# Kernel tuning notes

Hardware: AMD Instinct MI355X
Metric: run time of the kernel (lower is better)

Reference implementation:

```python
import jax, jax.numpy as jnp
import numpy as np

E = 1024      # d_model
H = 16        # num heads
D = E // H    # head dim = 64
FF = 4096     # dim_feedforward
WIN = 128
EPS = 1e-5    # layer-norm eps
NEG = -1e9


def setup_inputs() -> dict:
    key = jax.random.key(0)
    ks = jax.random.split(key, 16)
    s = 0.02
    f32 = jnp.float32
    return {
        "src":       jax.random.normal(ks[0], (2, 2048, E), f32),
        "in_proj_w": jax.random.normal(ks[1], (3 * E, E), f32) * s,
        "in_proj_b": jnp.zeros((3 * E,), f32),
        "out_w":     jax.random.normal(ks[2], (E, E), f32) * s,
        "out_b":     jnp.zeros((E,), f32),
        "lin1_w":    jax.random.normal(ks[3], (FF, E), f32) * s,
        "lin1_b":    jnp.zeros((FF,), f32),
        "lin2_w":    jax.random.normal(ks[4], (E, FF), f32) * s,
        "lin2_b":    jnp.zeros((E,), f32),
        "ln1_g":     jnp.ones((E,), f32),
        "ln1_beta":  jnp.zeros((E,), f32),
        "ln2_g":     jnp.ones((E,), f32),
        "ln2_beta":  jnp.zeros((E,), f32),
    }


def _layer_norm(x, g, b):
    mu = x.mean(-1, keepdims=True)
    var = ((x - mu) ** 2).mean(-1, keepdims=True)
    return (x - mu) * jax.lax.rsqrt(var + EPS) * g + b


def reference(src, in_proj_w, in_proj_b, out_w, out_b,
              lin1_w, lin1_b, lin2_w, lin2_b,
              ln1_g, ln1_beta, ln2_g, ln2_beta):
    B, L, _ = src.shape  # batch_first=True
    x = src

    # fused QKV projection (torch Linear: y = x @ W.T + b)
    qkv = x @ in_proj_w.T + in_proj_b            # [B, L, 3E]
    q, k, v = jnp.split(qkv, 3, axis=-1)
    q = q.reshape(B, L, H, D)
    k = k.reshape(B, L, H, D)
    v = v.reshape(B, L, H, D)

    scores = jnp.einsum('blhd,bmhd->bhlm', q, k) / np.float32(np.sqrt(D))
    idx = jnp.arange(L)
    band = jnp.abs(idx[:, None] - idx[None, :]) <= WIN   # [L, L] allowed positions
    scores = jnp.where(band, scores, NEG)
    attn = jax.nn.softmax(scores, axis=-1)

    ctx = jnp.einsum('bhlm,bmhd->blhd', attn, v).reshape(B, L, E)
    attn_out = ctx @ out_w.T + out_b

    # post-norm transformer encoder layer (norm_first=False default)
    x = _layer_norm(x + attn_out, ln1_g, ln1_beta)
    ff = jax.nn.relu(x @ lin1_w.T + lin1_b) @ lin2_w.T + lin2_b
    return _layer_norm(x + ff, ln2_g, ln2_beta)
```

## Files before the change

### kernel.cpp

```cpp
#include <hip/hip_runtime.h>
#include <cstdint>
#include <cstddef>


typedef __attribute__((ext_vector_type(8))) short short8;
typedef __attribute__((ext_vector_type(4))) float f32x4;

__device__ __forceinline__ float b2f(unsigned short u) {
  union { unsigned int i; float f; } x; x.i = ((unsigned int)u) << 16; return x.f;
}
__device__ __forceinline__ unsigned short f2b(float f) {
  union { float f; unsigned int i; } x; x.f = f;
  unsigned int i = x.i;
  unsigned int r = (i + 0x7FFFu + ((i >> 16) & 1u)) >> 16;
  return (unsigned short)r;
}
__device__ __forceinline__ uint4 pack8(float4 f0, float4 f1) {
  uint4 r;
  r.x = (unsigned)f2b(f0.x) | ((unsigned)f2b(f0.y) << 16);
  r.y = (unsigned)f2b(f0.z) | ((unsigned)f2b(f0.w) << 16);
  r.z = (unsigned)f2b(f1.x) | ((unsigned)f2b(f1.y) << 16);
  r.w = (unsigned)f2b(f1.z) | ((unsigned)f2b(f1.w) << 16);
  return r;
}

__device__ __forceinline__ void gl_lds16(const unsigned short* g, unsigned short* l) {
  __builtin_amdgcn_global_load_lds(
      (const __attribute__((address_space(1))) unsigned int*)g,
      (__attribute__((address_space(3))) unsigned int*)l, 16, 0, 0);
}

__global__ __launch_bounds__(256) void conv_k(
    const float* __restrict__ in, unsigned short* __restrict__ out, int n)
{
  const int i = (blockIdx.x * 256 + threadIdx.x) * 8;
  if (i < n) {
    const float4 f0 = *(const float4*)(in + i);
    const float4 f1 = *(const float4*)(in + i + 4);
    *(uint4*)(out + i) = pack8(f0, f1);
  }
}

__global__ __launch_bounds__(256) void conv3_k(
    const float* __restrict__ src, unsigned short* __restrict__ srcb,
    const float* __restrict__ w_in, const float* __restrict__ w_out,
    unsigned short* __restrict__ wslot)
{
  const int i = (blockIdx.x * 256 + threadIdx.x) * 8;
  const float* in;
  unsigned short* out;
  if (i < 4194304)      { in = src + i;                 out = srcb + i; }
  else if (i < 7340032) { in = w_in + (i - 4194304);    out = wslot + (i - 4194304); }
  else                  { in = w_out + (i - 7340032);   out = wslot + (i - 4194304); }
  const float4 f0 = *(const float4*)(in);
  const float4 f1 = *(const float4*)(in + 4);
  *(uint4*)(out) = pack8(f0, f1);
}

template<int RELU, int OUT32>
__global__ __launch_bounds__(512, 2) void gemm256(
    const unsigned short* __restrict__ A, const unsigned short* __restrict__ Wb,
    const float* __restrict__ bias, void* __restrict__ out,
    int M, int N, int K)
{
  __shared__ unsigned short As[2][256 * 64];
  __shared__ unsigned short Bs[2][256 * 64];

  const int tid = threadIdx.x;
  const int lane = tid & 63, wid = tid >> 6;
  const int wm = wid >> 2, wn = wid & 3;

  const int gx = gridDim.x;
  const int flat = blockIdx.y * gx + blockIdx.x;
  const int chunk = (gx * gridDim.y) >> 3;
  const int nf = (flat & 7) * chunk + (flat >> 3);
  const int m0 = (nf / gx) * 256, n0 = (nf % gx) * 256;

  int offA[2][2], offB[2][2], ldsO2[2][2];
#pragma unroll
  for (int h1 = 0; h1 < 2; ++h1)
#pragma unroll
    for (int i = 0; i < 2; ++i) {
      const int sl = i * 512 + tid;
      const int r = h1 * 128 + (sl >> 3);
      const int sslot = sl & 7;
      const int c = (sslot + r) & 7;
      offA[h1][i] = (m0 + r) * K + c * 8;
      offB[h1][i] = (n0 + r) * K + c * 8;
      ldsO2[h1][i] = (h1 * 1024 + i * 512 + (tid & ~63)) * 8;
    }

  const int cl = lane & 15;
  const int kg = lane >> 4;

  int aoff[4][2], boff[2][2];
#pragma unroll
  for (int mt = 0; mt < 4; ++mt) {
    const int ar = wm * 64 + mt * 16 + cl;
#pragma unroll
    for (int ks = 0; ks < 2; ++ks)
      aoff[mt][ks] = ar * 64 + (((ks * 4 + kg) - ar) & 7) * 8;
  }
#pragma unroll
  for (int nt = 0; nt < 2; ++nt) {
    const int br = wn * 32 + nt * 16 + cl;
#pragma unroll
    for (int ks = 0; ks < 2; ++ks)
      boff[nt][ks] = br * 64 + (((ks * 4 + kg) - br) & 7) * 8;
  }

  f32x4 acc[8][4];
#pragma unroll
  for (int i = 0; i < 8; ++i)
#pragma unroll
    for (int j = 0; j < 4; ++j) acc[i][j] = (f32x4){0.f, 0.f, 0.f, 0.f};

  const int steps = K >> 6;

#define STAGE256(idx_) do { const int _x = (idx_); if (_x < 4 * steps) {        \
    const int T_ = _x >> 2, j_ = _x & 3, bf_ = T_ & 1; const int ko = T_ << 6;  \
    if (j_ == 0)      { gl_lds16(A  + offA[0][0] + ko, &As[bf_][ldsO2[0][0]]);  \
                        gl_lds16(A  + offA[0][1] + ko, &As[bf_][ldsO2[0][1]]); }\
    else if (j_ == 1) { gl_lds16(Wb + offB[0][0] + ko, &Bs[bf_][ldsO2[0][0]]);  \
                        gl_lds16(Wb + offB[0][1] + ko, &Bs[bf_][ldsO2[0][1]]); }\
    else if (j_ == 2) { gl_lds16(Wb + offB[1][0] + ko, &Bs[bf_][ldsO2[1][0]]);  \
                        gl_lds16(Wb + offB[1][1] + ko, &Bs[bf_][ldsO2[1][1]]); }\
    else              { gl_lds16(A  + offA[1][0] + ko, &As[bf_][ldsO2[1][0]]);  \
                        gl_lds16(A  + offA[1][1] + ko, &As[bf_][ldsO2[1][1]]); }\
  } } while (0)

  STAGE256(0); STAGE256(1); STAGE256(2); STAGE256(3);
  STAGE256(4); STAGE256(5); STAGE256(6);
  asm volatile("s_waitcnt vmcnt(6)" ::: "memory");
  __builtin_amdgcn_s_barrier();

  int cur = 0;
  for (int s = 0; s < steps; ++s) {
    short8 bf0[2][2], af[4][2];
#pragma unroll
    for (int nt = 0; nt < 2; ++nt)
#pragma unroll
      for (int ks = 0; ks < 2; ++ks) bf0[nt][ks] = *(const short8*)&Bs[cur][boff[nt][ks]];
#pragma unroll
    for (int mt = 0; mt < 4; ++mt)
#pragma unroll
      for (int ks = 0; ks < 2; ++ks) af[mt][ks] = *(const short8*)&As[cur][aoff[mt][ks]];
    STAGE256(4 * s + 7);
    asm volatile("s_waitcnt lgkmcnt(8)" ::: "memory");
    __builtin_amdgcn_s_barrier();
    asm volatile("s_waitcnt lgkmcnt(0)" ::: "memory");
    __builtin_amdgcn_sched_barrier(0);
    __builtin_amdgcn_s_setprio(1);
#pragma unroll
    for (int mt = 0; mt < 4; ++mt)
#pragma unroll
      for (int nt = 0; nt < 2; ++nt)
#pragma unroll
        for (int ks = 0; ks < 2; ++ks)
          acc[mt][nt] = __builtin_amdgcn_mfma_f32_16x16x32_bf16(af[mt][ks], bf0[nt][ks], acc[mt][nt], 0, 0, 0);
    __builtin_amdgcn_s_setprio(0);
    __builtin_amdgcn_s_barrier();

    short8 bf1[2][2];
#pragma unroll
    for (int nt = 0; nt < 2; ++nt)
#pragma unroll
      for (int ks = 0; ks < 2; ++ks) bf1[nt][ks] = *(const short8*)&Bs[cur][boff[nt][ks] + 8192];
    STAGE256(4 * s + 8);
    __builtin_amdgcn_s_barrier();
    asm volatile("s_waitcnt lgkmcnt(0)" ::: "memory");
    __builtin_amdgcn_sched_barrier(0);
    __builtin_amdgcn_s_setprio(1);
#pragma unroll
    for (int mt = 0; mt < 4; ++mt)
#pragma unroll
      for (int nt = 0; nt < 2; ++nt)
#pragma unroll
        for (int ks = 0; ks < 2; ++ks)
          acc[mt][nt + 2] = __builtin_amdgcn_mfma_f32_16x16x32_bf16(af[mt][ks], bf1[nt][ks], acc[mt][nt + 2], 0, 0, 0);
    __builtin_amdgcn_s_setprio(0);
    __builtin_amdgcn_s_barrier();

    short8 ag[4][2];
#pragma unroll
    for (int mt = 0; mt < 4; ++mt)
#pragma unroll
      for (int ks = 0; ks < 2; ++ks) ag[mt][ks] = *(const short8*)&As[cur][aoff[mt][ks] + 8192];
    STAGE256(4 * s + 9);
    __builtin_amdgcn_s_barrier();
    asm volatile("s_waitcnt lgkmcnt(0)" ::: "memory");
    __builtin_amdgcn_sched_barrier(0);
    __builtin_amdgcn_s_setprio(1);
#pragma unroll
    for (int mt = 0; mt < 4; ++mt)
#pragma unroll
      for (int nt = 0; nt < 2; ++nt)
#pragma unroll
        for (int ks = 0; ks < 2; ++ks)
          acc[mt + 4][nt] = __builtin_amdgcn_mfma_f32_16x16x32_bf16(ag[mt][ks], bf0[nt][ks], acc[mt + 4][nt], 0, 0, 0);
    __builtin_amdgcn_s_setprio(0);
    __builtin_amdgcn_s_barrier();

    STAGE256(4 * s + 10);
    if (s < steps - 2)       asm volatile("s_waitcnt vmcnt(6)" ::: "memory");
    else if (s == steps - 2) asm volatile("s_waitcnt vmcnt(0)" ::: "memory");
    __builtin_amdgcn_s_barrier();
    __builtin_amdgcn_s_setprio(1);
#pragma unroll
    for (int mt = 0; mt < 4; ++mt)
#pragma unroll
      for (int nt = 0; nt < 2; ++nt)
#pragma unroll
        for (int ks = 0; ks < 2; ++ks)
          acc[mt + 4][nt + 2] = __builtin_amdgcn_mfma_f32_16x16x32_bf16(ag[mt][ks], bf1[nt][ks], acc[mt + 4][nt + 2], 0, 0, 0);
    __builtin_amdgcn_s_setprio(0);
    __builtin_amdgcn_s_barrier();

    cur ^= 1;
  }
#undef STAGE256

#pragma unroll
  for (int nt = 0; nt < 4; ++nt) {
    const int colB = wn * 32 + (nt & 1) * 16 + (nt >> 1) * 128;
    const int col = n0 + colB + cl;
    const float bvs = bias[col];
#pragma unroll
    for (int mt = 0; mt < 8; ++mt) {
      const int rowA = wm * 64 + (mt & 3) * 16 + (mt >> 2) * 128;
#pragma unroll
      for (int r = 0; r < 4; ++r) {
        const int grow = m0 + rowA + kg * 4 + r;
        float v = acc[mt][nt][r] + bvs;
        if (RELU) v = fmaxf(v, 0.f);
        if (OUT32) ((float*)out)[(size_t)grow * N + col] = v;
        else       ((unsigned short*)out)[(size_t)grow * N + col] = f2b(v);
      }
    }
  }
}

template<int OUT32>
__global__ __launch_bounds__(256) void gemm64(
    const unsigned short* __restrict__ A, const unsigned short* __restrict__ Wb,
    const float* __restrict__ bias, void* __restrict__ out,
    int M, int N, int K)
{
  __shared__ unsigned short As[3][64 * 64];
  __shared__ unsigned short Bs[3][128 * 64];

  const int tid = threadIdx.x;
  const int lane = tid & 63, wid = tid >> 6;

  const int nwgx = gridDim.x;
  const int flat = blockIdx.y * nwgx + blockIdx.x;
  const int chunk = (nwgx * gridDim.y) >> 3;
  const int nf = (flat & 7) * chunk + (flat >> 3);
  const int m0 = (nf / nwgx) * 64, n0 = (nf % nwgx) * 128;

  const unsigned short* gA[2];
  const unsigned short* gW[4];
  int ldsA[2], ldsB[4];
#pragma unroll
  for (int i = 0; i < 2; ++i) {
    const int sl = wid * 128 + i * 64 + lane;
    const int r = sl >> 3, s = sl & 7, c = (s + r) & 7;
    gA[i] = A + (size_t)(m0 + r) * K + c * 8;
    ldsA[i] = (wid * 128 + i * 64) * 8;
  }
#pragma unroll
  for (int i = 0; i < 4; ++i) {
    const int sl = wid * 256 + i * 64 + lane;
    const int r = sl >> 3, s = sl & 7, c = (s + r) & 7;
    gW[i] = Wb + (size_t)(n0 + r) * K + c * 8;
    ldsB[i] = (wid * 256 + i * 64) * 8;
  }

  const int cl = lane & 15;
  const int kg = lane >> 4;
  int aoff[4][2], boff[2][2];
#pragma unroll
  for (int t = 0; t < 4; ++t) {
    const int ar = t * 16 + cl;
#pragma unroll
    for (int ks = 0; ks < 2; ++ks)
      aoff[t][ks] = ar * 64 + ((ks * 4 + kg - ar) & 7) * 8;
  }
#pragma unroll
  for (int t = 0; t < 2; ++t) {
    const int br = wid * 32 + t * 16 + cl;
#pragma unroll
    for (int ks = 0; ks < 2; ++ks)
      boff[t][ks] = br * 64 + ((ks * 4 + kg - br) & 7) * 8;
  }

  f32x4 acc[4][2];
#pragma unroll
  for (int i = 0; i < 4; ++i)
#pragma unroll
    for (int j = 0; j < 2; ++j) acc[i][j] = (f32x4){0.f, 0.f, 0.f, 0.f};

  const int steps = K >> 6;

  const int pre = steps < 3 ? steps : 3;
  for (int t = 0; t < pre; ++t) {
#pragma unroll
    for (int i = 0; i < 2; ++i) { gl_lds16(gA[i], &As[t][ldsA[i]]); gA[i] += 64; }
#pragma unroll
    for (int i = 0; i < 4; ++i) { gl_lds16(gW[i], &Bs[t][ldsB[i]]); gW[i] += 64; }
  }

  int cur = 0;
  for (int s = 0; s < steps; ++s) {
    const int rem = steps - 1 - s;
    if (rem >= 2)      asm volatile("s_waitcnt vmcnt(12)" ::: "memory");
    else if (rem == 1) asm volatile("s_waitcnt vmcnt(6)" ::: "memory");
    else               asm volatile("s_waitcnt vmcnt(0)" ::: "memory");
    __builtin_amdgcn_s_barrier();

    short8 af[4][2], bf[2][2];
#pragma unroll
    for (int t = 0; t < 4; ++t)
#pragma unroll
      for (int ks = 0; ks < 2; ++ks) af[t][ks] = *(const short8*)&As[cur][aoff[t][ks]];
#pragma unroll
    for (int t = 0; t < 2; ++t)
#pragma unroll
      for (int ks = 0; ks < 2; ++ks) bf[t][ks] = *(const short8*)&Bs[cur][boff[t][ks]];

    asm volatile("s_waitcnt lgkmcnt(0)" ::: "memory");
    __builtin_amdgcn_sched_barrier(0);
    __builtin_amdgcn_s_barrier();

    if (s + 3 < steps) {
#pragma unroll
      for (int i = 0; i < 2; ++i) { gl_lds16(gA[i], &As[cur][ldsA[i]]); gA[i] += 64; }
#pragma unroll
      for (int i = 0; i < 4; ++i) { gl_lds16(gW[i], &Bs[cur][ldsB[i]]); gW[i] += 64; }
    }

#pragma unroll
    for (int mt = 0; mt < 4; ++mt)
#pragma unroll
      for (int nt = 0; nt < 2; ++nt)
#pragma unroll
        for (int ks = 0; ks < 2; ++ks)
          acc[mt][nt] = __builtin_amdgcn_mfma_f32_16x16x32_bf16(af[mt][ks], bf[nt][ks], acc[mt][nt], 0, 0, 0);

    cur = (cur == 2) ? 0 : cur + 1;
  }

#pragma unroll
  for (int nt = 0; nt < 2; ++nt) {
    const int col = n0 + wid * 32 + nt * 16 + cl;
    const float bvs = bias[col];
#pragma unroll
    for (int mt = 0; mt < 4; ++mt) {
#pragma unroll
      for (int r = 0; r < 4; ++r) {
        const int grow = m0 + mt * 16 + kg * 4 + r;
        const float v = acc[mt][nt][r] + bvs;
        if (OUT32) ((float*)out)[(size_t)grow * N + col] = v;
        else       ((unsigned short*)out)[(size_t)grow * N + col] = f2b(v);
      }
    }
  }
}

__global__ __launch_bounds__(256) void attn_mfma(
    const unsigned short* __restrict__ qkv, unsigned short* __restrict__ ctx)
{
  __shared__ unsigned short Ks[64 * 72];
  __shared__ unsigned short Vt[64 * 72];
  __shared__ unsigned short Ps[64 * 72];

  const int tid = threadIdx.x;
  const int bid = blockIdx.x;
  const int qt = bid & 31, h = (bid >> 5) & 15, b = bid >> 9;
  const int q0 = qt * 64;
  const int wstart = max(0, q0 - 128);
  const int wend = min(2048, q0 + 64 + 128);
  const int ntile = (wend - wstart + 63) >> 6;
  const size_t rowb = (size_t)b * 2048;

  const int lane = tid & 63, wid = tid >> 6;
  const int cl = lane & 15;
  const int kq = (lane >> 4) * 8;
  const int rowg = lane >> 4;

  short8 aQ[2];
#pragma unroll
  for (int ks = 0; ks < 2; ++ks)
    aQ[ks] = *(const short8*)(qkv + (rowb + q0 + wid * 16 + cl) * 3072 + h * 64 + ks * 32 + kq);

  float m_i[4], l_i[4];
  f32x4 O[4];
#pragma unroll
  for (int r = 0; r < 4; ++r) { m_i[r] = -1.0e30f; l_i[r] = 0.f; }
#pragma unroll
  for (int nt = 0; nt < 4; ++nt) O[nt] = (f32x4){0.f, 0.f, 0.f, 0.f};

  for (int t = 0; t < ntile; ++t) {
    const int jbase = wstart + t * 64;
    __syncthreads();
    for (int idx = tid; idx < 512; idx += 256) {
      const int r = idx >> 3, c = idx & 7;
      const int jg = jbase + r;
      uint4 kv = {0u, 0u, 0u, 0u}, vv = {0u, 0u, 0u, 0u};
      if (jg < wend) {
        const size_t base = (rowb + jg) * 3072 + h * 64 + c * 8;
        kv = *(const uint4*)(qkv + base + 1024);
        vv = *(const uint4*)(qkv + base + 2048);
      }
      *(uint4*)&Ks[r * 72 + c * 8] = kv;
      const unsigned short* vs = (const unsigned short*)&vv;
#pragma unroll
      for (int ii = 0; ii < 8; ++ii) Vt[(c * 8 + ii) * 72 + r] = vs[ii];
    }
    __syncthreads();

    f32x4 S[4];
#pragma unroll
    for (int nt = 0; nt < 4; ++nt) S[nt] = (f32x4){0.f, 0.f, 0.f, 0.f};
#pragma unroll
    for (int nt = 0; nt < 4; ++nt)
#pragma unroll
      for (int ks = 0; ks < 2; ++ks) {
        const short8 bK = *(const short8*)&Ks[(nt * 16 + cl) * 72 + ks * 32 + kq];
        S[nt] = __builtin_amdgcn_mfma_f32_16x16x32_bf16(aQ[ks], bK, S[nt], 0, 0, 0);
      }

    float sc[4][4];
#pragma unroll
    for (int nt = 0; nt < 4; ++nt) {
      const int jg = jbase + nt * 16 + cl;
#pragma unroll
      for (int r = 0; r < 4; ++r) {
        const int i = q0 + wid * 16 + rowg * 4 + r;
        const bool v = (jg < wend) && (jg >= i - 128) && (jg <= i + 128);
        sc[nt][r] = v ? S[nt][r] * 0.125f : -1.0e30f;
      }
    }

    float alpha[4], p[4][4];
#pragma unroll
    for (int r = 0; r < 4; ++r) {
      float tm = fmaxf(fmaxf(sc[0][r], sc[1][r]), fmaxf(sc[2][r], sc[3][r]));
      tm = fmaxf(tm, __shfl_xor(tm, 1, 64));
      tm = fmaxf(tm, __shfl_xor(tm, 2, 64));
      tm = fmaxf(tm, __shfl_xor(tm, 4, 64));
      tm = fmaxf(tm, __shfl_xor(tm, 8, 64));
      const float mn = fmaxf(m_i[r], tm);
      alpha[r] = __expf(m_i[r] - mn);
      m_i[r] = mn;
      float ps = 0.f;
#pragma unroll
      for (int nt = 0; nt < 4; ++nt) { p[nt][r] = __expf(sc[nt][r] - mn); ps += p[nt][r]; }
      ps += __shfl_xor(ps, 1, 64);
      ps += __shfl_xor(ps, 2, 64);
      ps += __shfl_xor(ps, 4, 64);
      ps += __shfl_xor(ps, 8, 64);
      l_i[r] = l_i[r] * alpha[r] + ps;
    }

#pragma unroll
    for (int nt = 0; nt < 4; ++nt)
#pragma unroll
      for (int r = 0; r < 4; ++r)
        Ps[(wid * 16 + rowg * 4 + r) * 72 + nt * 16 + cl] = f2b(p[nt][r]);
    __syncthreads();

#pragma unroll
    for (int nt = 0; nt < 4; ++nt)
#pragma unroll
      for (int r = 0; r < 4; ++r) O[nt][r] *= alpha[r];
    short8 aP[2];
#pragma unroll
    for (int ks = 0; ks < 2; ++ks)
      aP[ks] = *(const short8*)&Ps[(wid * 16 + cl) * 72 + ks * 32 + kq];
#pragma unroll
    for (int nt = 0; nt < 4; ++nt)
#pragma unroll
      for (int ks = 0; ks < 2; ++ks) {
        const short8 bV = *(const short8*)&Vt[(nt * 16 + cl) * 72 + ks * 32 + kq];
        O[nt] = __builtin_amdgcn_mfma_f32_16x16x32_bf16(aP[ks], bV, O[nt], 0, 0, 0);
      }
  }

#pragma unroll
  for (int nt = 0; nt < 4; ++nt) {
    const int d = nt * 16 + cl;
#pragma unroll
    for (int r = 0; r < 4; ++r) {
      const int i = q0 + wid * 16 + rowg * 4 + r;
      ctx[(rowb + i) * 1024 + h * 64 + d] = f2b(O[nt][r] / l_i[r]);
    }
  }
}

template<int AF32, int BF32, int OF32>
__global__ __launch_bounds__(256) void ln_k(
    const void* __restrict__ a, const void* __restrict__ b,
    const float* __restrict__ g, const float* __restrict__ be,
    void* __restrict__ o)
{
  __shared__ float rbuf[8];
  const int tid = threadIdx.x;
  const size_t base = (size_t)blockIdx.x * 1024;
  const int lane = tid & 63, wid = tid >> 6;

  float xv[4], s = 0.f, sq = 0.f;
#pragma unroll
  for (int t = 0; t < 4; ++t) {
    const int c = tid + t * 256;
    const float av = AF32 ? ((const float*)a)[base + c]
                          : b2f(((const unsigned short*)a)[base + c]);
    const float bv = BF32 ? ((const float*)b)[base + c]
                          : b2f(((const unsigned short*)b)[base + c]);
    const float x = av + bv;
    xv[t] = x; s += x; sq += x * x;
  }
  for (int o2 = 1; o2 < 64; o2 <<= 1) { s += __shfl_xor(s, o2, 64); sq += __shfl_xor(sq, o2, 64); }
  if (lane == 0) { rbuf[wid] = s; rbuf[wid + 4] = sq; }
  __syncthreads();
  s  = rbuf[0] + rbuf[1] + rbuf[2] + rbuf[3];
  sq = rbuf[4] + rbuf[5] + rbuf[6] + rbuf[7];
  const float mean = s * (1.0f / 1024.f);
  const float var = sq * (1.0f / 1024.f) - mean * mean;
  const float rstd = rsqrtf(var + 1e-5f);
#pragma unroll
  for (int t = 0; t < 4; ++t) {
    const int c = tid + t * 256;
    const float y = (xv[t] - mean) * rstd * g[c] + be[c];
    if (OF32) ((float*)o)[base + c] = y;
    else      ((unsigned short*)o)[base + c] = f2b(y);
  }
}

extern "C" void kernel_launch(void* const* d_in, const int* in_sizes, int n_in,
                              void* d_out, int out_size, void* d_ws, size_t ws_size,
                              hipStream_t stream)
{
  (void)in_sizes; (void)n_in; (void)out_size; (void)ws_size;
  const float* src   = (const float*)d_in[0];
  const float* w_in  = (const float*)d_in[1];
  const float* b_in  = (const float*)d_in[2];
  const float* w_out = (const float*)d_in[3];
  const float* b_out = (const float*)d_in[4];
  const float* w1    = (const float*)d_in[5];
  const float* b1    = (const float*)d_in[6];
  const float* w2    = (const float*)d_in[7];
  const float* b2    = (const float*)d_in[8];
  const float* g1    = (const float*)d_in[9];
  const float* be1   = (const float*)d_in[10];
  const float* g2    = (const float*)d_in[11];
  const float* be2   = (const float*)d_in[12];

  char* ws = (char*)d_ws;
  unsigned short* srcb  = (unsigned short*)(ws);
  unsigned short* x1b   = srcb;
  unsigned short* qkv   = (unsigned short*)(ws + 8388608);
  unsigned short* ctx   = (unsigned short*)(ws + 33554432);
  unsigned short* attnb = (unsigned short*)(ws + 8388608);
  unsigned short* ff1   = (unsigned short*)(ws + 8388608);
  unsigned short* wslot = (unsigned short*)(ws + 41943040);
  float*          outf  = (float*)d_out;

  conv3_k<<<dim3(4096), 256, 0, stream>>>(src, srcb, w_in, w_out, wslot);
  gemm256<0, 0><<<dim3(12, 16), 512, 0, stream>>>(srcb, wslot, b_in, qkv, 4096, 3072, 1024);
  attn_mfma<<<dim3(1024), 256, 0, stream>>>(qkv, ctx);
  gemm64<0><<<dim3(8, 64), 256, 0, stream>>>(ctx, wslot + 3145728, b_out, attnb, 4096, 1024, 1024);
  ln_k<0, 0, 0><<<dim3(4096), 256, 0, stream>>>(srcb, attnb, g1, be1, x1b);
  conv_k<<<dim3(2048), 256, 0, stream>>>(w1, wslot, 4194304);
  gemm256<1, 0><<<dim3(16, 16), 512, 0, stream>>>(x1b, wslot, b1, ff1, 4096, 4096, 1024);
  conv_k<<<dim3(2048), 256, 0, stream>>>(w2, wslot, 4194304);
  gemm64<1><<<dim3(8, 64), 256, 0, stream>>>(ff1, wslot, b2, outf, 4096, 1024, 4096);
  ln_k<0, 1, 1><<<dim3(4096), 256, 0, stream>>>(x1b, outf, g2, be2, outf);
}
```

Before: 305.9 us.

## Merge weight conversions, restructure gemm64 prefetch, emit bf16 FF2 output

The two separate FP32-to-bf16 weight conversion launches are merged into one kernel, with the lin2 weights staged temporarily in the output buffer. The gemm64 main loop now keeps a 2-deep prefetch issued right after the barrier into the next buffer, which removes the second barrier per K step. The final FF2 GEMM writes bf16 into scratch instead of fp32, and layer norm reads that bf16 buffer. The aims are fewer launches, less synchronisation and less output traffic, at the cost of a shallower prefetch and bf16 rounding of the FF2 result.

```diff
diff --git a/kernel.cpp b/kernel.cpp
--- a/kernel.cpp
+++ b/kernel.cpp
@@ -30,17 +30,6 @@
       (__attribute__((address_space(3))) unsigned int*)l, 16, 0, 0);
 }
 
-__global__ __launch_bounds__(256) void conv_k(
-    const float* __restrict__ in, unsigned short* __restrict__ out, int n)
-{
-  const int i = (blockIdx.x * 256 + threadIdx.x) * 8;
-  if (i < n) {
-    const float4 f0 = *(const float4*)(in + i);
-    const float4 f1 = *(const float4*)(in + i + 4);
-    *(uint4*)(out + i) = pack8(f0, f1);
-  }
-}
-
 __global__ __launch_bounds__(256) void conv3_k(
     const float* __restrict__ src, unsigned short* __restrict__ srcb,
     const float* __restrict__ w_in, const float* __restrict__ w_out,
@@ -52,6 +41,20 @@
   if (i < 4194304)      { in = src + i;                 out = srcb + i; }
   else if (i < 7340032) { in = w_in + (i - 4194304);    out = wslot + (i - 4194304); }
   else                  { in = w_out + (i - 7340032);   out = wslot + (i - 4194304); }
+  const float4 f0 = *(const float4*)(in);
+  const float4 f1 = *(const float4*)(in + 4);
+  *(uint4*)(out) = pack8(f0, f1);
+}
+
+__global__ __launch_bounds__(256) void conv2_k(
+    const float* __restrict__ w1, unsigned short* __restrict__ o1,
+    const float* __restrict__ w2, unsigned short* __restrict__ o2)
+{
+  const int i = (blockIdx.x * 256 + threadIdx.x) * 8;
+  const float* in;
+  unsigned short* out;
+  if (i < 4194304) { in = w1 + i;             out = o1 + i; }
+  else             { in = w2 + (i - 4194304); out = o2 + (i - 4194304); }
   const float4 f0 = *(const float4*)(in);
   const float4 f1 = *(const float4*)(in + 4);
   *(uint4*)(out) = pack8(f0, f1);
@@ -302,7 +305,7 @@
 
   const int steps = K >> 6;
 
-  const int pre = steps < 3 ? steps : 3;
+  const int pre = steps < 2 ? steps : 2;
   for (int t = 0; t < pre; ++t) {
 #pragma unroll
     for (int i = 0; i < 2; ++i) { gl_lds16(gA[i], &As[t][ldsA[i]]); gA[i] += 64; }
@@ -310,13 +313,17 @@
     for (int i = 0; i < 4; ++i) { gl_lds16(gW[i], &Bs[t][ldsB[i]]); gW[i] += 64; }
   }
 
-  int cur = 0;
+  int cur = 0, nxt = 2;
   for (int s = 0; s < steps; ++s) {
-    const int rem = steps - 1 - s;
-    if (rem >= 2)      asm volatile("s_waitcnt vmcnt(12)" ::: "memory");
-    else if (rem == 1) asm volatile("s_waitcnt vmcnt(6)" ::: "memory");
+    if (s + 1 < steps) asm volatile("s_waitcnt vmcnt(6)" ::: "memory");
     else               asm volatile("s_waitcnt vmcnt(0)" ::: "memory");
     __builtin_amdgcn_s_barrier();
+    if (s + 2 < steps) {
+#pragma unroll
+      for (int i = 0; i < 2; ++i) { gl_lds16(gA[i], &As[nxt][ldsA[i]]); gA[i] += 64; }
+#pragma unroll
+      for (int i = 0; i < 4; ++i) { gl_lds16(gW[i], &Bs[nxt][ldsB[i]]); gW[i] += 64; }
+    }
 
     short8 af[4][2], bf[2][2];
 #pragma unroll
@@ -330,14 +337,6 @@
 
     asm volatile("s_waitcnt lgkmcnt(0)" ::: "memory");
     __builtin_amdgcn_sched_barrier(0);
-    __builtin_amdgcn_s_barrier();
-
-    if (s + 3 < steps) {
-#pragma unroll
-      for (int i = 0; i < 2; ++i) { gl_lds16(gA[i], &As[cur][ldsA[i]]); gA[i] += 64; }
-#pragma unroll
-      for (int i = 0; i < 4; ++i) { gl_lds16(gW[i], &Bs[cur][ldsB[i]]); gW[i] += 64; }
-    }
 
 #pragma unroll
     for (int mt = 0; mt < 4; ++mt)
@@ -348,6 +347,7 @@
           acc[mt][nt] = __builtin_amdgcn_mfma_f32_16x16x32_bf16(af[mt][ks], bf[nt][ks], acc[mt][nt], 0, 0, 0);
 
     cur = (cur == 2) ? 0 : cur + 1;
+    nxt = (nxt == 2) ? 0 : nxt + 1;
   }
 
 #pragma unroll
@@ -565,15 +565,15 @@
   unsigned short* ff1   = (unsigned short*)(ws + 8388608);
   unsigned short* wslot = (unsigned short*)(ws + 41943040);
   float*          outf  = (float*)d_out;
+  unsigned short* w2b   = (unsigned short*)d_out;
 
   conv3_k<<<dim3(4096), 256, 0, stream>>>(src, srcb, w_in, w_out, wslot);
   gemm256<0, 0><<<dim3(12, 16), 512, 0, stream>>>(srcb, wslot, b_in, qkv, 4096, 3072, 1024);
   attn_mfma<<<dim3(1024), 256, 0, stream>>>(qkv, ctx);
   gemm64<0><<<dim3(8, 64), 256, 0, stream>>>(ctx, wslot + 3145728, b_out, attnb, 4096, 1024, 1024);
   ln_k<0, 0, 0><<<dim3(4096), 256, 0, stream>>>(srcb, attnb, g1, be1, x1b);
-  conv_k<<<dim3(2048), 256, 0, stream>>>(w1, wslot, 4194304);
+  conv2_k<<<dim3(4096), 256, 0, stream>>>(w1, wslot, w2, w2b);
   gemm256<1, 0><<<dim3(16, 16), 512, 0, stream>>>(x1b, wslot, b1, ff1, 4096, 4096, 1024);
-  conv_k<<<dim3(2048), 256, 0, stream>>>(w2, wslot, 4194304);
-  gemm64<1><<<dim3(8, 64), 256, 0, stream>>>(ff1, wslot, b2, outf, 4096, 1024, 4096);
-  ln_k<0, 1, 1><<<dim3(4096), 256, 0, stream>>>(x1b, outf, g2, be2, outf);
-}
+  gemm64<0><<<dim3(8, 64), 256, 0, stream>>>(ff1, w2b, b2, wslot, 4096, 1024, 4096);
+  ln_k<0, 0, 1><<<dim3(4096), 256, 0, stream>>>(x1b, wslot, g2, be2, outf);
+}
```

Result: no change. 311.8 us (+1.9%).
